# Performance work log

Measured on AMD Instinct MI355X. Metric: run time of the kernel, lower is better.

The kernel has to match this reference:

```python
import jax, jax.numpy as jnp
import numpy as np

LOG2E = 1.4426950408889634  # 1/ln(2): convert natural-log gates to log2 space (kernel uses exp2)
BT = 64  # chunk size


def setup_inputs() -> dict:
    key = jax.random.key(0)
    ks = jax.random.split(key, 5)
    B, H, T, K, V = 4, 8, 4096, 128, 128
    return {
        "q": jax.random.normal(ks[0], (B, H, T, K), dtype=jnp.float32),
        "k": jax.random.normal(ks[1], (B, H, T, K), dtype=jnp.float32),
        "v": jax.random.normal(ks[2], (B, H, T, V), dtype=jnp.float32),
        "i_gate": jax.random.normal(ks[3], (B, H, T), dtype=jnp.float32),
        "f_gate": jax.random.normal(ks[4], (B, H, T), dtype=jnp.float32),
    }


def reference(q, k, v, i_gate, f_gate):
    B, H, T, K = q.shape
    V = v.shape[-1]
    NT = T // BT
    scale = K ** -0.5

    # gate preprocessing: log-sigmoid forget gate, both gates moved to log2 space
    vecF = jax.nn.log_sigmoid(f_gate) * LOG2E  # [B,H,T]
    vecI = i_gate * LOG2E                      # [B,H,T]

    f_c = vecF.reshape(B, H, NT, BT)
    i_c = vecI.reshape(B, H, NT, BT)
    qc = q.reshape(B, H, NT, BT, K)
    kc = k.reshape(B, H, NT, BT, K)
    vc = v.reshape(B, H, NT, BT, V)

    vecB = jnp.cumsum(f_c, axis=-1)            # inclusive cumsum of f within chunk [B,H,NT,BT]
    scaG = vecB[..., -1]                       # total decay per chunk [B,H,NT]
    vecA = i_c + (scaG[..., None] - vecB)      # i_j + sum of f after j within chunk

    # ---- inter-chunk recurrence over matrix state C, normalizer n, max m ----
    kx = jnp.moveaxis(kc, 2, 0)  # [NT,B,H,BT,K]
    vx = jnp.moveaxis(vc, 2, 0)
    ax = jnp.moveaxis(vecA, 2, 0)  # [NT,B,H,BT]
    gx = jnp.moveaxis(scaG, 2, 0)  # [NT,B,H]

    C0 = jnp.zeros((B, H, K, V), dtype=q.dtype)
    n0 = jnp.zeros((B, H, K), dtype=q.dtype)
    m0 = jnp.zeros((B, H), dtype=q.dtype)

    def step(carry, inp):
        C, n, m = carry
        kk, vv, a, g = inp
        m_next = jnp.maximum(g + m, jnp.max(a, axis=-1))      # running stabilizer max
        dec = jnp.exp2(g + m - m_next)                        # [B,H]
        kbar = kk * jnp.exp2(a - m_next[..., None])[..., None]
        C_next = C * dec[..., None, None] + jnp.einsum('bhtk,bhtv->bhkv', kbar, vv)
        n_next = n * dec[..., None] + kbar.sum(axis=-2)
        return (C_next, n_next, m_next), (C, n, m)

    _, (Cp, np_, mp) = jax.lax.scan(step, (C0, n0, m0), (kx, vx, ax, gx))
    Cp = jnp.moveaxis(Cp, 0, 2)   # state entering each chunk [B,H,NT,K,V]
    np_ = jnp.moveaxis(np_, 0, 2)  # [B,H,NT,K]
    mp = jnp.moveaxis(mp, 0, 2)   # [B,H,NT]

    # ---- intra-chunk parallel part ----
    idx = jnp.arange(BT)
    causal = idx[:, None] >= idx[None, :]  # query i attends key j<=i
    # logD[i,j] = B_i - B_j + I_j for j<=i
    logD = vecB[..., :, None] - vecB[..., None, :] + i_c[..., None, :]
    logD = jnp.where(causal, logD, -jnp.inf)
    m_intra = logD.max(axis=-1)                                   # [B,H,NT,BT]
    m_comb = jnp.maximum(mp[..., None] + vecB, m_intra)           # total stabilizer per row
    D = jnp.exp2(logD - m_comb[..., None])                        # masked entries -> 0

    S = jnp.einsum('bhcik,bhcjk->bhcij', qc, kc) * scale * D
    qbar = qc * (scale * jnp.exp2(vecB + mp[..., None] - m_comb))[..., None]

    Hnum = jnp.einsum('bhcik,bhckv->bhciv', qbar, Cp) + jnp.einsum('bhcij,bhcjv->bhciv', S, vc)
    den = jnp.einsum('bhcik,bhck->bhci', qbar, np_) + S.sum(axis=-1)
    norm = jnp.maximum(jnp.abs(den), jnp.exp2(-m_comb))
    h = Hnum / norm[..., None]
    return h.reshape(B, H, T, V)
```

## Files before the change

kernel.cpp:

```cpp
#include <hip/hip_runtime.h>
#include <hip/hip_bf16.h>
#include <math.h>


#define LOG2E 1.4426950408889634f
constexpr int Bsz = 4, Hsz = 8, Tsz = 4096, Ksz = 128, Vsz = 128;
constexpr int BT = 64, NT = 64, BH = Bsz * Hsz;
constexpr float SCALE = 0.08838834764831845f;
constexpr int GS = 8, NG = NT / GS;

typedef __attribute__((ext_vector_type(8))) short short8v;
typedef __attribute__((ext_vector_type(4))) float f32x4;
typedef __attribute__((ext_vector_type(4))) unsigned short u16x4;
typedef __attribute__((ext_vector_type(8))) unsigned short u16x8;

__device__ inline float bf2f(unsigned short u) {
    union { unsigned int i; float f; } c; c.i = ((unsigned int)u) << 16; return c.f;
}
__device__ inline unsigned short f2bf(float f) {
    __hip_bfloat16 h = __float2bfloat16(f);
    union { __hip_bfloat16 b; unsigned short u; } cv; cv.b = h; return cv.u;
}
__device__ inline float f4c(const float4& v, int y) {
    return y == 0 ? v.x : y == 1 ? v.y : y == 2 ? v.z : v.w;
}

__global__ __launch_bounds__(64) void k_gates(
    const float* __restrict__ ig, const float* __restrict__ fg,
    float* __restrict__ vecB, float* __restrict__ vecI, float* __restrict__ vecA,
    float* __restrict__ mintra, float* __restrict__ scaG, float* __restrict__ scaA)
{
    int c = blockIdx.x, bh = blockIdx.y, lane = threadIdx.x;
    int t = bh * Tsz + c * BT + lane;
    float f = fg[t];
    float ls = fminf(f, 0.f) - log1pf(expf(-fabsf(f)));
    float vF = ls * LOG2E;
    float vI = ig[t] * LOG2E;
    float b = vF;
    #pragma unroll
    for (int off = 1; off < 64; off <<= 1) {
        float o = __shfl_up(b, off, 64);
        if (lane >= off) b += o;
    }
    float g = __shfl(b, 63, 64);
    float mi = vI - b;
    #pragma unroll
    for (int off = 1; off < 64; off <<= 1) {
        float o = __shfl_up(mi, off, 64);
        if (lane >= off) mi = fmaxf(mi, o);
    }
    float a = vI + g - b;
    vecB[t] = b; vecI[t] = vI; vecA[t] = a; mintra[t] = b + mi;
    float am = a;
    #pragma unroll
    for (int off = 32; off; off >>= 1) am = fmaxf(am, __shfl_xor(am, off, 64));
    if (lane == 0) { scaG[bh * NT + c] = g; scaA[bh * NT + c] = am; }
}

__global__ __launch_bounds__(64) void k_mscan(
    const float* __restrict__ scaG, const float* __restrict__ scaA,
    float* __restrict__ mp, float* __restrict__ dec,
    float* __restrict__ pdec, float* __restrict__ decG)
{
    int bh = blockIdx.x, lane = threadIdx.x;
    float g0 = scaG[bh * NT + lane];
    float a = g0, b = scaA[bh * NT + lane];
    #pragma unroll
    for (int off = 1; off < 64; off <<= 1) {
        float ap = __shfl_up(a, off, 64);
        float bp = __shfl_up(b, off, 64);
        if (lane >= off) { b = fmaxf(bp + a, b); a = ap + a; }
    }
    float m_incl = fmaxf(a, b);
    float m_prev = __shfl_up(m_incl, 1, 64);
    if (lane == 0) { m_prev = 0.f; mp[bh * (NT + 1)] = 0.f; }
    mp[bh * (NT + 1) + lane + 1] = m_incl;
    dec[bh * NT + lane] = exp2f(g0 + m_prev - m_incl);
    float cumE = a - g0;
    int gs = lane & ~(GS - 1);
    float cumE_gs = __shfl(cumE, gs, 64);
    float mp_gs   = __shfl(m_prev, gs, 64);
    pdec[bh * NT + lane] = exp2f(cumE - cumE_gs + mp_gs - m_prev);
    int ge = (lane * GS) & 63, gl = (lane * GS + GS - 1) & 63;
    float cumS = __shfl(cumE, ge, 64);
    float mS   = __shfl(m_prev, ge, 64);
    float cumL = __shfl(a, gl, 64);
    float mL   = __shfl(m_incl, gl, 64);
    if (lane < NG) decG[bh * NG + lane] = exp2f(cumL - cumS + mS - mL);
}

__global__ __launch_bounds__(256, 2) void k_state(
    const float* __restrict__ kg, const float* __restrict__ vg,
    const float* __restrict__ vecA, const float* __restrict__ mp,
    const float* __restrict__ dec,
    unsigned short* __restrict__ CpL, unsigned short* __restrict__ Gb,
    float* __restrict__ npl, float* __restrict__ nG)
{
    int g = blockIdx.x, bh = blockIdx.y, vhalf = blockIdx.z, tid = threadIdx.x;
    int c0 = g * GS;
    int lane = tid & 63, wid = tid >> 6;
    int lrow = lane & 15, kgrp = lane >> 4;

    __shared__ __align__(16) unsigned short kT[2][128][72];
    __shared__ __align__(16) unsigned short vT[2][64][72];
    __shared__ float nUp[2][128][5];

    int cb = tid & 15, jr = tid >> 4;
    int wboff = (((jr >> 1) ^ (cb & 7)) * 16) + (jr & 1) * 8;
    const float* mpb = mp + bh * (NT + 1);

    float4 kreg[4][2], vreg[4];
    auto issue_loads = [&](int cc) {
        size_t hbc = (size_t)bh * Tsz + (size_t)(c0 + cc) * BT;
        #pragma unroll
        for (int x = 0; x < 4; ++x) {
            #pragma unroll
            for (int p = 0; p < 2; ++p)
                kreg[x][p] = *(const float4*)(kg + (hbc + jr * 4 + x) * Ksz + p * 64 + cb * 4);
            vreg[x] = *(const float4*)(vg + (hbc + jr * 4 + x) * Vsz + vhalf * 64 + cb * 4);
        }
    };
    auto cvt_store = [&](int cc, int bb) {
        size_t hbc = (size_t)bh * Tsz + (size_t)(c0 + cc) * BT;
        float mpn = mpb[c0 + cc + 1];
        float s4[4];
        #pragma unroll
        for (int x = 0; x < 4; ++x) s4[x] = exp2f(vecA[hbc + jr * 4 + x] - mpn);
        #pragma unroll
        for (int p = 0; p < 2; ++p) {
            int cc0 = p * 64 + cb * 4;
            #pragma unroll
            for (int y = 0; y < 4; ++y) {
                u16x4 h;
                float psum = 0.f;
                #pragma unroll
                for (int x = 0; x < 4; ++x) {
                    float kf = f4c(kreg[x][p], y) * s4[x];
                    h[x] = f2bf(kf);
                    psum += kf;
                }
                *(u16x4*)((char*)&kT[bb][cc0 + y][0] + wboff) = h;
                psum += __shfl_xor(psum, 16, 64);
                psum += __shfl_xor(psum, 32, 64);
                if (kgrp == 0) nUp[bb][cc0 + y][wid] = psum;
            }
        }
        #pragma unroll
        for (int y = 0; y < 4; ++y) {
            u16x4 w;
            #pragma unroll
            for (int x = 0; x < 4; ++x) w[x] = f2bf(f4c(vreg[x], y));
            *(u16x4*)((char*)&vT[bb][cb * 4 + y][0] + wboff) = w;
        }
    };

    issue_loads(0);
    cvt_store(0, 0);
    __syncthreads();

    f32x4 acc[2][4];
    #pragma unroll
    for (int kt = 0; kt < 2; ++kt)
        #pragma unroll
        for (int vt = 0; vt < 4; ++vt) acc[kt][vt] = (f32x4){0.f, 0.f, 0.f, 0.f};
    float n_own = 0.f;

    int bb = 0;
    for (int t = 0; t < GS; ++t) {
        if (t + 1 < GS) issue_loads(t + 1);
        int c = c0 + t;
        if (t > 0) {
            unsigned short* Cb = CpL + (size_t)(bh * NT + c) * (Ksz * Vsz);
            #pragma unroll
            for (int kt = 0; kt < 2; ++kt) {
                int ktile = wid * 2 + kt;
                #pragma unroll
                for (int vt = 0; vt < 4; ++vt) {
                    u16x4 w;
                    #pragma unroll
                    for (int r = 0; r < 4; ++r) w[r] = f2bf(acc[kt][vt][r]);
                    *(u16x4*)(Cb + ((size_t)(ktile * 8 + vhalf * 4 + vt) * 64 + lane) * 4) = w;
                }
            }
        }
        if (vhalf == 0 && tid < Ksz) npl[(size_t)(bh * NT + c) * Ksz + tid] = n_own;
        float dct = dec[bh * NT + c];
        #pragma unroll
        for (int kt = 0; kt < 2; ++kt)
            #pragma unroll
            for (int vt = 0; vt < 4; ++vt)
                #pragma unroll
                for (int r = 0; r < 4; ++r) acc[kt][vt][r] *= dct;
        #pragma unroll
        for (int ks = 0; ks < 2; ++ks) {
            int G2 = ks * 4 + kgrp;
            #pragma unroll
            for (int kt = 0; kt < 2; ++kt) {
                int arow = (wid * 2 + kt) * 16 + lrow;
                short8v af = *(const short8v*)((const char*)&kT[bb][arow][0]
                                               + ((G2 ^ ((arow >> 2) & 7)) * 16));
                #pragma unroll
                for (int vt = 0; vt < 4; ++vt) {
                    int brow = vt * 16 + lrow;
                    short8v bv = *(const short8v*)((const char*)&vT[bb][brow][0]
                                                   + ((G2 ^ ((brow >> 2) & 7)) * 16));
                    acc[kt][vt] = __builtin_amdgcn_mfma_f32_16x16x32_bf16(af, bv, acc[kt][vt], 0, 0, 0);
                }
            }
        }
        if (tid < Ksz) {
            float s = nUp[bb][tid][0] + nUp[bb][tid][1] + nUp[bb][tid][2] + nUp[bb][tid][3];
            n_own = n_own * dct + s;
        }
        if (t + 1 < GS) {
            cvt_store(t + 1, bb ^ 1);
            __syncthreads();
            bb ^= 1;
        }
    }
    unsigned short* Gg = Gb + (size_t)(bh * NG + g) * (Ksz * Vsz);
    #pragma unroll
    for (int kt = 0; kt < 2; ++kt) {
        int ktile = wid * 2 + kt;
        #pragma unroll
        for (int vt = 0; vt < 4; ++vt) {
            u16x4 w;
            #pragma unroll
            for (int r = 0; r < 4; ++r) w[r] = f2bf(acc[kt][vt][r]);
            *(u16x4*)(Gg + ((size_t)(ktile * 8 + vhalf * 4 + vt) * 64 + lane) * 4) = w;
        }
    }
    if (vhalf == 0 && tid < Ksz) nG[(size_t)(bh * NG + g) * Ksz + tid] = n_own;
}

__global__ __launch_bounds__(128) void k_gscan(
    unsigned short* __restrict__ Gb, float* __restrict__ nG,
    const float* __restrict__ decG)
{
    int s = blockIdx.x, bh = blockIdx.y, tid = threadIdx.x;
    __shared__ float dgs[NG];
    if (tid < NG) dgs[tid] = decG[bh * NG + tid];
    __syncthreads();
    if (s == 32) {
        float n = 0.f;
        size_t base = (size_t)bh * NG * Ksz + tid;
        #pragma unroll
        for (int g = 0; g < NG; ++g) {
            float u = nG[base + (size_t)g * Ksz];
            nG[base + (size_t)g * Ksz] = n;
            n = n * dgs[g] + u;
        }
        return;
    }
    size_t base = (size_t)bh * NG * (Ksz * Vsz) + s * 512 + tid * 4;
    float C0 = 0.f, C1 = 0.f, C2 = 0.f, C3 = 0.f;
    #pragma unroll
    for (int g = 0; g < NG; ++g) {
        size_t idx = base + (size_t)g * (Ksz * Vsz);
        u16x4 u = *(const u16x4*)(Gb + idx);
        u16x4 w;
        w.x = f2bf(C0); w.y = f2bf(C1); w.z = f2bf(C2); w.w = f2bf(C3);
        *(u16x4*)(Gb + idx) = w;
        float d = dgs[g];
        C0 = C0 * d + bf2f(u.x); C1 = C1 * d + bf2f(u.y);
        C2 = C2 * d + bf2f(u.z); C3 = C3 * d + bf2f(u.w);
    }
}

__global__ __launch_bounds__(256, 2) void k_intra(
    const float* __restrict__ qg, const float* __restrict__ kgl, const float* __restrict__ vg,
    const float* __restrict__ vecB, const float* __restrict__ vecI,
    const float* __restrict__ mintra, const float* __restrict__ mp,
    const float* __restrict__ npl, const float* __restrict__ nB,
    const unsigned short* __restrict__ CpL, const unsigned short* __restrict__ Bb,
    const float* __restrict__ pdec, float* __restrict__ out)
{
    int b0 = blockIdx.x, bh = blockIdx.y, tid = threadIdx.x;
    int c = ((b0 & 7) << 3) | (b0 >> 3);
    int lane = tid & 63, wid = tid >> 6;
    int lrow = lane & 15, kgrp = lane >> 4;
    int grp = c / GS;
    bool firstc = (c & (GS - 1)) == 0;

    __shared__ __align__(16) unsigned short R[17408];
    __shared__ float rowf[BT], colf[BT], sfqs[BT], emcs[BT], denb[BT], npv[Ksz];

    auto khi = (unsigned short(*)[136])R;
    auto klo = (unsigned short(*)[136])(R + 64 * 136);
    auto Sb  = (unsigned short(*)[72])R;
    unsigned short* vTf = R + 64 * 72;
    unsigned short* cpsF = R;

    size_t hb = (size_t)bh * Tsz + (size_t)c * BT;
    float mpc = mp[bh * (NT + 1) + c];
    float pd = pdec[bh * NT + c];
    if (tid < BT) {
        float b = vecB[hb + tid];
        float mc = fmaxf(mpc + b, mintra[hb + tid]);
        rowf[tid] = SCALE * exp2f(b - mc);
        colf[tid] = exp2f(vecI[hb + tid] - b);
        sfqs[tid] = SCALE * exp2f(b + mpc - mc);
        emcs[tid] = exp2f(-mc);
    }
    if (tid < Ksz)
        npv[tid] = npl[((size_t)bh * NT + c) * Ksz + tid]
                 + pd * nB[((size_t)bh * NG + grp) * Ksz + tid];

    const float4* k4 = (const float4*)(kgl + hb * Ksz);
    for (int e = tid; e < BT * Ksz / 4; e += 256) {
        int i = e >> 5, c4 = (e & 31) * 4;
        float4 kv = k4[e];
        u16x4 h, l;
        h.x = f2bf(kv.x); l.x = f2bf(kv.x - bf2f(h.x));
        h.y = f2bf(kv.y); l.y = f2bf(kv.y - bf2f(h.y));
        h.z = f2bf(kv.z); l.z = f2bf(kv.z - bf2f(h.z));
        h.w = f2bf(kv.w); l.w = f2bf(kv.w - bf2f(h.w));
        *(u16x4*)&khi[i][c4] = h; *(u16x4*)&klo[i][c4] = l;
    }
    const float* qrow = qg + (hb + wid * 16 + lrow) * Ksz;
    float qf[4][8];
    #pragma unroll
    for (int ks = 0; ks < 4; ++ks) {
        float4 a = *(const float4*)(qrow + ks * 32 + kgrp * 8);
        float4 b = *(const float4*)(qrow + ks * 32 + kgrp * 8 + 4);
        qf[ks][0] = a.x; qf[ks][1] = a.y; qf[ks][2] = a.z; qf[ks][3] = a.w;
        qf[ks][4] = b.x; qf[ks][5] = b.y; qf[ks][6] = b.z; qf[ks][7] = b.w;
    }
    int vcb = tid & 15, jb = tid >> 4;
    float vpre[2][4][4];
    #pragma unroll
    for (int p = 0; p < 2; ++p)
        #pragma unroll
        for (int x = 0; x < 4; ++x) {
            float4 r4 = *(const float4*)(vg + (hb + jb * 4 + x) * Vsz + p * 64 + vcb * 4);
            vpre[p][x][0] = r4.x; vpre[p][x][1] = r4.y; vpre[p][x][2] = r4.z; vpre[p][x][3] = r4.w;
        }
    __syncthreads();

    float dot = 0.f;
    #pragma unroll
    for (int ks = 0; ks < 4; ++ks)
        #pragma unroll
        for (int x = 0; x < 8; ++x) dot += qf[ks][x] * npv[ks * 32 + kgrp * 8 + x];
    dot += __shfl_xor(dot, 16, 64);
    dot += __shfl_xor(dot, 32, 64);
    float qdot = sfqs[wid * 16 + lrow] * dot;

    short8v qh[4], ql[4];
    #pragma unroll
    for (int ks = 0; ks < 4; ++ks)
        #pragma unroll
        for (int x = 0; x < 8; ++x) {
            float f = qf[ks][x];
            unsigned short hh = f2bf(f);
            qh[ks][x] = (short)hh;
            ql[ks][x] = (short)f2bf(f - bf2f(hh));
        }

    f32x4 accS[4];
    #pragma unroll
    for (int jt = 0; jt < 4; ++jt) accS[jt] = (f32x4){0.f, 0.f, 0.f, 0.f};
    #pragma unroll
    for (int ks = 0; ks < 4; ++ks) {
        #pragma unroll
        for (int jt = 0; jt < 4; ++jt) {
            if (jt <= wid) {
                short8v bh_ = *(const short8v*)&khi[jt * 16 + lrow][ks * 32 + kgrp * 8];
                short8v bl  = *(const short8v*)&klo[jt * 16 + lrow][ks * 32 + kgrp * 8];
                accS[jt] = __builtin_amdgcn_mfma_f32_16x16x32_bf16(qh[ks], bh_, accS[jt], 0, 0, 0);
                accS[jt] = __builtin_amdgcn_mfma_f32_16x16x32_bf16(ql[ks], bh_, accS[jt], 0, 0, 0);
                accS[jt] = __builtin_amdgcn_mfma_f32_16x16x32_bf16(qh[ks], bl,  accS[jt], 0, 0, 0);
            }
        }
    }

    float rsum[4] = {0.f, 0.f, 0.f, 0.f};
    unsigned short sreg[4][4];
    #pragma unroll
    for (int jt = 0; jt < 4; ++jt)
        #pragma unroll
        for (int r = 0; r < 4; ++r) {
            int i = wid * 16 + kgrp * 4 + r, j = jt * 16 + lrow;
            float val = (j <= i) ? accS[jt][r] * rowf[i] * colf[j] : 0.f;
            rsum[r] += val;
            sreg[jt][r] = f2bf(val);
        }
    #pragma unroll
    for (int r = 0; r < 4; ++r) {
        rsum[r] += __shfl_xor(rsum[r], 1, 64);
        rsum[r] += __shfl_xor(rsum[r], 2, 64);
        rsum[r] += __shfl_xor(rsum[r], 4, 64);
        rsum[r] += __shfl_xor(rsum[r], 8, 64);
    }
    float qd[4];
    #pragma unroll
    for (int r = 0; r < 4; ++r) qd[r] = __shfl(qdot, kgrp * 4 + r, 64);
    if (lrow == 0) {
        #pragma unroll
        for (int r = 0; r < 4; ++r) {
            int i = wid * 16 + kgrp * 4 + r;
            float den = qd[r] + rsum[r];
            denb[i] = 1.f / fmaxf(fabsf(den), emcs[i]);
        }
    }
    __syncthreads();

    const u16x8* Cg = (const u16x8*)(CpL + ((size_t)bh * NT + c) * (Ksz * Vsz));
    const u16x8* Bg = (const u16x8*)(Bb + ((size_t)bh * NG + grp) * (Ksz * Vsz));
    u16x8 cpre[8], bpre[8];
    #pragma unroll
    for (int p2 = 0; p2 < 8; ++p2) bpre[p2] = Bg[tid + p2 * 256];
    if (!firstc) {
        #pragma unroll
        for (int p2 = 0; p2 < 8; ++p2) cpre[p2] = Cg[tid + p2 * 256];
    }

    #pragma unroll
    for (int jt = 0; jt < 4; ++jt)
        #pragma unroll
        for (int r = 0; r < 4; ++r)
            Sb[wid * 16 + kgrp * 4 + r][jt * 16 + lrow] = sreg[jt][r];
    #pragma unroll
    for (int p = 0; p < 2; ++p)
        #pragma unroll
        for (int y = 0; y < 4; ++y) {
            int row = p * 64 + vcb * 4 + y;
            int swzb = (jb * 8) ^ ((row & 7) << 4);
            u16x4 w;
            #pragma unroll
            for (int x = 0; x < 4; ++x) w[x] = f2bf(vpre[p][x][y]);
            *(u16x4*)((char*)(vTf + row * 64) + swzb) = w;
        }
    __syncthreads();

    f32x4 accV[8];
    #pragma unroll
    for (int vt = 0; vt < 8; ++vt) accV[vt] = (f32x4){0.f, 0.f, 0.f, 0.f};
    #pragma unroll
    for (int ks = 0; ks < 2; ++ks) {
        short8v as_ = *(const short8v*)&Sb[wid * 16 + lrow][ks * 32 + kgrp * 8];
        #pragma unroll
        for (int vt = 0; vt < 8; ++vt) {
            int row = vt * 16 + lrow;
            int swzb = ((ks * 64 + kgrp * 16)) ^ ((row & 7) << 4);
            short8v bv = *(const short8v*)((const char*)(vTf + row * 64) + swzb);
            accV[vt] = __builtin_amdgcn_mfma_f32_16x16x32_bf16(as_, bv, accV[vt], 0, 0, 0);
        }
    }
    __syncthreads();

    if (firstc) {
        #pragma unroll
        for (int p2 = 0; p2 < 8; ++p2) {
            int idx = tid + p2 * 256;
            *(u16x8*)&cpsF[idx * 8] = bpre[p2];
        }
    } else {
        #pragma unroll
        for (int p2 = 0; p2 < 8; ++p2) {
            int idx = tid + p2 * 256;
            u16x8 cv = cpre[p2], bv = bpre[p2];
            u16x8 w;
            #pragma unroll
            for (int e = 0; e < 8; ++e) w[e] = f2bf(bf2f(cv[e]) + pd * bf2f(bv[e]));
            *(u16x8*)&cpsF[idx * 8] = w;
        }
    }
    __syncthreads();

    f32x4 accC[8];
    #pragma unroll
    for (int vt = 0; vt < 8; ++vt) accC[vt] = (f32x4){0.f, 0.f, 0.f, 0.f};
    #pragma unroll
    for (int ks = 0; ks < 4; ++ks) {
        int ktile = ks * 2 + (kgrp >> 1);
        int lsrc = (kgrp & 1) * 32 + lrow;
        #pragma unroll
        for (int vt = 0; vt < 8; ++vt) {
            const unsigned short* pf = &cpsF[((ktile * 8 + vt) * 64 + lsrc) * 4];
            u16x4 lo4 = *(const u16x4*)pf;
            u16x4 hi4 = *(const u16x4*)(pf + 64);
            short8v bc;
            bc[0] = (short)lo4.x; bc[1] = (short)lo4.y; bc[2] = (short)lo4.z; bc[3] = (short)lo4.w;
            bc[4] = (short)hi4.x; bc[5] = (short)hi4.y; bc[6] = (short)hi4.z; bc[7] = (short)hi4.w;
            accC[vt] = __builtin_amdgcn_mfma_f32_16x16x32_bf16(qh[ks], bc, accC[vt], 0, 0, 0);
            accC[vt] = __builtin_amdgcn_mfma_f32_16x16x32_bf16(ql[ks], bc, accC[vt], 0, 0, 0);
        }
    }
    size_t gb = hb * Vsz;
    #pragma unroll
    for (int vt = 0; vt < 8; ++vt)
        #pragma unroll
        for (int r = 0; r < 4; ++r) {
            int i = wid * 16 + kgrp * 4 + r, vc = vt * 16 + lrow;
            out[gb + (size_t)i * Vsz + vc] = (sfqs[i] * accC[vt][r] + accV[vt][r]) * denb[i];
        }
}

extern "C" void kernel_launch(void* const* d_in, const int* in_sizes, int n_in,
                              void* d_out, int out_size, void* d_ws, size_t ws_size,
                              hipStream_t stream) {
    const float* q  = (const float*)d_in[0];
    const float* k  = (const float*)d_in[1];
    const float* v  = (const float*)d_in[2];
    const float* ig = (const float*)d_in[3];
    const float* fg = (const float*)d_in[4];
    float* out = (float*)d_out;

    float* ws = (float*)d_ws;
    float* vecB   = ws;
    float* vecI   = vecB + BH * Tsz;
    float* vecA   = vecI + BH * Tsz;
    float* mintra = vecA + BH * Tsz;
    float* scaG   = mintra + BH * Tsz;
    float* scaA   = scaG + BH * NT;
    float* dec    = scaA + BH * NT;
    float* pdec   = dec + BH * NT;
    float* decG   = pdec + BH * NT;
    float* mp     = decG + BH * NG;
    float* npl    = mp + BH * (NT + 1);
    float* nG     = npl + BH * NT * Ksz;
    unsigned short* CpL = (unsigned short*)(nG + BH * NG * Ksz);
    unsigned short* Gb  = CpL + (size_t)BH * NT * Ksz * Vsz;

    k_gates<<<dim3(NT, BH), 64, 0, stream>>>(ig, fg, vecB, vecI, vecA, mintra, scaG, scaA);
    k_mscan<<<dim3(BH), 64, 0, stream>>>(scaG, scaA, mp, dec, pdec, decG);
    k_state<<<dim3(NG, BH, 2), 256, 0, stream>>>(k, v, vecA, mp, dec, CpL, Gb, npl, nG);
    k_gscan<<<dim3(33, BH), 128, 0, stream>>>(Gb, nG, decG);
    k_intra<<<dim3(NT, BH), 256, 0, stream>>>(q, k, v, vecB, vecI, mintra, mp,
                                              npl, nG, CpL, Gb, pdec, out);
}
```

Before: 112.4 us.

## Split k_state work across K halves to double block count

The state-accumulation kernel now splits the K dimension into two halves in addition to the V halves, launching four blocks per (group, head) instead of two. Each block holds one K-tile per wave, so it uses half the accumulators, half the k staging in shared memory and half the k loads. The aim is more parallelism and occupancy (NG*BH*2 = 512 blocks was small for the GPU). In exchange, every block now reloads and converts the same v tile, doubling v traffic and conversion work.

```diff
diff --git a/kernel.cpp b/kernel.cpp
--- a/kernel.cpp
+++ b/kernel.cpp
@@ -96,27 +96,26 @@
     unsigned short* __restrict__ CpL, unsigned short* __restrict__ Gb,
     float* __restrict__ npl, float* __restrict__ nG)
 {
-    int g = blockIdx.x, bh = blockIdx.y, vhalf = blockIdx.z, tid = threadIdx.x;
+    int g = blockIdx.x, bh = blockIdx.y, q4 = blockIdx.z, tid = threadIdx.x;
+    int khalf = q4 >> 1, vhalf = q4 & 1;
     int c0 = g * GS;
     int lane = tid & 63, wid = tid >> 6;
     int lrow = lane & 15, kgrp = lane >> 4;
 
-    __shared__ __align__(16) unsigned short kT[2][128][72];
+    __shared__ __align__(16) unsigned short kT[2][64][72];
     __shared__ __align__(16) unsigned short vT[2][64][72];
-    __shared__ float nUp[2][128][5];
+    __shared__ float nUp[2][64][5];
 
     int cb = tid & 15, jr = tid >> 4;
     int wboff = (((jr >> 1) ^ (cb & 7)) * 16) + (jr & 1) * 8;
     const float* mpb = mp + bh * (NT + 1);
 
-    float4 kreg[4][2], vreg[4];
+    float4 kreg[4], vreg[4];
     auto issue_loads = [&](int cc) {
         size_t hbc = (size_t)bh * Tsz + (size_t)(c0 + cc) * BT;
         #pragma unroll
         for (int x = 0; x < 4; ++x) {
-            #pragma unroll
-            for (int p = 0; p < 2; ++p)
-                kreg[x][p] = *(const float4*)(kg + (hbc + jr * 4 + x) * Ksz + p * 64 + cb * 4);
+            kreg[x] = *(const float4*)(kg + (hbc + jr * 4 + x) * Ksz + khalf * 64 + cb * 4);
             vreg[x] = *(const float4*)(vg + (hbc + jr * 4 + x) * Vsz + vhalf * 64 + cb * 4);
         }
     };
@@ -127,30 +126,22 @@
         #pragma unroll
         for (int x = 0; x < 4; ++x) s4[x] = exp2f(vecA[hbc + jr * 4 + x] - mpn);
         #pragma unroll
-        for (int p = 0; p < 2; ++p) {
-            int cc0 = p * 64 + cb * 4;
-            #pragma unroll
-            for (int y = 0; y < 4; ++y) {
-                u16x4 h;
-                float psum = 0.f;
-                #pragma unroll
-                for (int x = 0; x < 4; ++x) {
-                    float kf = f4c(kreg[x][p], y) * s4[x];
-                    h[x] = f2bf(kf);
-                    psum += kf;
-                }
-                *(u16x4*)((char*)&kT[bb][cc0 + y][0] + wboff) = h;
-                psum += __shfl_xor(psum, 16, 64);
-                psum += __shfl_xor(psum, 32, 64);
-                if (kgrp == 0) nUp[bb][cc0 + y][wid] = psum;
+        for (int y = 0; y < 4; ++y) {
+            int row = cb * 4 + y;
+            u16x4 h, w;
+            float psum = 0.f;
+            #pragma unroll
+            for (int x = 0; x < 4; ++x) {
+                float kf = f4c(kreg[x], y) * s4[x];
+                h[x] = f2bf(kf);
+                psum += kf;
+                w[x] = f2bf(f4c(vreg[x], y));
             }
-        }
-        #pragma unroll
-        for (int y = 0; y < 4; ++y) {
-            u16x4 w;
-            #pragma unroll
-            for (int x = 0; x < 4; ++x) w[x] = f2bf(f4c(vreg[x], y));
-            *(u16x4*)((char*)&vT[bb][cb * 4 + y][0] + wboff) = w;
+            *(u16x4*)((char*)&kT[bb][row][0] + wboff) = h;
+            *(u16x4*)((char*)&vT[bb][row][0] + wboff) = w;
+            psum += __shfl_xor(psum, 16, 64);
+            psum += __shfl_xor(psum, 32, 64);
+            if (kgrp == 0) nUp[bb][row][wid] = psum;
         }
     };
 
@@ -158,11 +149,9 @@
     cvt_store(0, 0);
     __syncthreads();
 
-    f32x4 acc[2][4];
-    #pragma unroll
-    for (int kt = 0; kt < 2; ++kt)
-        #pragma unroll
-        for (int vt = 0; vt < 4; ++vt) acc[kt][vt] = (f32x4){0.f, 0.f, 0.f, 0.f};
+    f32x4 acc[4];
+    #pragma unroll
+    for (int vt = 0; vt < 4; ++vt) acc[vt] = (f32x4){0.f, 0.f, 0.f, 0.f};
     float n_own = 0.f;
 
     int bb = 0;
@@ -171,44 +160,37 @@
         int c = c0 + t;
         if (t > 0) {
             unsigned short* Cb = CpL + (size_t)(bh * NT + c) * (Ksz * Vsz);
-            #pragma unroll
-            for (int kt = 0; kt < 2; ++kt) {
-                int ktile = wid * 2 + kt;
+            int kt_g = khalf * 4 + wid;
+            #pragma unroll
+            for (int vt = 0; vt < 4; ++vt) {
+                int vt_g = vhalf * 4 + vt;
+                u16x4 w;
                 #pragma unroll
-                for (int vt = 0; vt < 4; ++vt) {
-                    u16x4 w;
-                    #pragma unroll
-                    for (int r = 0; r < 4; ++r) w[r] = f2bf(acc[kt][vt][r]);
-                    *(u16x4*)(Cb + ((size_t)(ktile * 8 + vhalf * 4 + vt) * 64 + lane) * 4) = w;
-                }
+                for (int r = 0; r < 4; ++r) w[r] = f2bf(acc[vt][r]);
+                *(u16x4*)(Cb + ((size_t)(kt_g * 8 + vt_g) * 64 + lane) * 4) = w;
             }
         }
-        if (vhalf == 0 && tid < Ksz) npl[(size_t)(bh * NT + c) * Ksz + tid] = n_own;
+        if (vhalf == 0 && tid < 64) npl[(size_t)(bh * NT + c) * Ksz + khalf * 64 + tid] = n_own;
         float dct = dec[bh * NT + c];
         #pragma unroll
-        for (int kt = 0; kt < 2; ++kt)
-            #pragma unroll
-            for (int vt = 0; vt < 4; ++vt)
-                #pragma unroll
-                for (int r = 0; r < 4; ++r) acc[kt][vt][r] *= dct;
+        for (int vt = 0; vt < 4; ++vt)
+            #pragma unroll
+            for (int r = 0; r < 4; ++r) acc[vt][r] *= dct;
         #pragma unroll
         for (int ks = 0; ks < 2; ++ks) {
             int G2 = ks * 4 + kgrp;
-            #pragma unroll
-            for (int kt = 0; kt < 2; ++kt) {
-                int arow = (wid * 2 + kt) * 16 + lrow;
-                short8v af = *(const short8v*)((const char*)&kT[bb][arow][0]
-                                               + ((G2 ^ ((arow >> 2) & 7)) * 16));
-                #pragma unroll
-                for (int vt = 0; vt < 4; ++vt) {
-                    int brow = vt * 16 + lrow;
-                    short8v bv = *(const short8v*)((const char*)&vT[bb][brow][0]
-                                                   + ((G2 ^ ((brow >> 2) & 7)) * 16));
-                    acc[kt][vt] = __builtin_amdgcn_mfma_f32_16x16x32_bf16(af, bv, acc[kt][vt], 0, 0, 0);
-                }
+            int arow = wid * 16 + lrow;
+            short8v af = *(const short8v*)((const char*)&kT[bb][arow][0]
+                                           + ((G2 ^ ((arow >> 2) & 7)) * 16));
+            #pragma unroll
+            for (int vt = 0; vt < 4; ++vt) {
+                int brow = vt * 16 + lrow;
+                short8v bv = *(const short8v*)((const char*)&vT[bb][brow][0]
+                                               + ((G2 ^ ((brow >> 2) & 7)) * 16));
+                acc[vt] = __builtin_amdgcn_mfma_f32_16x16x32_bf16(af, bv, acc[vt], 0, 0, 0);
             }
         }
-        if (tid < Ksz) {
+        if (tid < 64) {
             float s = nUp[bb][tid][0] + nUp[bb][tid][1] + nUp[bb][tid][2] + nUp[bb][tid][3];
             n_own = n_own * dct + s;
         }
@@ -219,18 +201,18 @@
         }
     }
     unsigned short* Gg = Gb + (size_t)(bh * NG + g) * (Ksz * Vsz);
-    #pragma unroll
-    for (int kt = 0; kt < 2; ++kt) {
-        int ktile = wid * 2 + kt;
+    {
+        int kt_g = khalf * 4 + wid;
         #pragma unroll
         for (int vt = 0; vt < 4; ++vt) {
+            int vt_g = vhalf * 4 + vt;
             u16x4 w;
             #pragma unroll
-            for (int r = 0; r < 4; ++r) w[r] = f2bf(acc[kt][vt][r]);
-            *(u16x4*)(Gg + ((size_t)(ktile * 8 + vhalf * 4 + vt) * 64 + lane) * 4) = w;
-        }
-    }
-    if (vhalf == 0 && tid < Ksz) nG[(size_t)(bh * NG + g) * Ksz + tid] = n_own;
+            for (int r = 0; r < 4; ++r) w[r] = f2bf(acc[vt][r]);
+            *(u16x4*)(Gg + ((size_t)(kt_g * 8 + vt_g) * 64 + lane) * 4) = w;
+        }
+    }
+    if (vhalf == 0 && tid < 64) nG[(size_t)(bh * NG + g) * Ksz + khalf * 64 + tid] = n_own;
 }
 
 __global__ __launch_bounds__(128) void k_gscan(
@@ -525,7 +507,7 @@
 
     k_gates<<<dim3(NT, BH), 64, 0, stream>>>(ig, fg, vecB, vecI, vecA, mintra, scaG, scaA);
     k_mscan<<<dim3(BH), 64, 0, stream>>>(scaG, scaA, mp, dec, pdec, decG);
-    k_state<<<dim3(NG, BH, 2), 256, 0, stream>>>(k, v, vecA, mp, dec, CpL, Gb, npl, nG);
+    k_state<<<dim3(NG, BH, 4), 256, 0, stream>>>(k, v, vecA, mp, dec, CpL, Gb, npl, nG);
     k_gscan<<<dim3(33, BH), 128, 0, stream>>>(Gb, nG, decG);
     k_intra<<<dim3(NT, BH), 256, 0, stream>>>(q, k, v, vecB, vecI, mintra, mp,
                                               npl, nG, CpL, Gb, pdec, out);
```

Result: slower. 117.1 us (+4.2%).
